# Performance work log

Measured on AMD Instinct MI355X. Metric: run time of the kernel, lower is better.

Reference implementation:

```python
import jax, jax.numpy as jnp
import numpy as np

B, D, L = 32, 512, 4096   # batch, latent_dim (dim1), time length
N, D2 = 77, 768           # text tokens, text_latent_dim (dim2)
BC = 24                   # number of conditioned batch elements
H = 8                     # num_heads
EPS = 1e-5


def _layernorm(x, g, b):
    mu = jnp.mean(x, axis=-1, keepdims=True)
    var = jnp.mean(jnp.square(x - mu), axis=-1, keepdims=True)
    return (x - mu) * jax.lax.rsqrt(var + EPS) * g + b


def setup_inputs() -> dict:
    key = jax.random.key(0)
    ks = jax.random.split(key, 8)
    s = 0.02
    return {
        "input_tensor": jax.random.normal(ks[0], (B, D, L), jnp.float32),
        "condition_tensor": jax.random.normal(ks[1], (B, N, D2), jnp.float32),
        "cond_indices": jnp.arange(BC, dtype=jnp.int64 if jax.config.jax_enable_x64 else jnp.int32),
        "ln_g": jnp.ones((D,), jnp.float32),
        "ln_b": jnp.zeros((D,), jnp.float32),
        "tln_g": jnp.ones((D2,), jnp.float32),
        "tln_b": jnp.zeros((D2,), jnp.float32),
        "Wq": jax.random.normal(ks[2], (D, D), jnp.float32) * s,
        "bq": jnp.zeros((D,), jnp.float32),
        "Wk": jax.random.normal(ks[3], (D2, D), jnp.float32) * s,
        "bk": jnp.zeros((D,), jnp.float32),
        "Wv": jax.random.normal(ks[4], (D2, D), jnp.float32) * s,
        "bv": jnp.zeros((D,), jnp.float32),
    }


def reference(input_tensor, condition_tensor, cond_indices,
              ln_g, ln_b, tln_g, tln_b, Wq, bq, Wk, bk, Wv, bv):
    dh = D // H
    # gather conditioned rows; [Bc, D, L] -> [Bc, T=L, D]
    x_cond = jnp.transpose(input_tensor[cond_indices], (0, 2, 1))
    cond = condition_tensor[cond_indices]  # [Bc, N, D2]

    q = _layernorm(x_cond, ln_g, ln_b) @ Wq + bq           # [Bc, T, D]
    cn = _layernorm(cond, tln_g, tln_b)                     # [Bc, N, D2]
    k = (cn @ Wk + bk).reshape(BC, N, H, dh)
    v = (cn @ Wv + bv).reshape(BC, N, H, dh)

    q = jax.nn.softmax(q.reshape(BC, L, H, dh), axis=-1)   # feature-map softmax
    k = jax.nn.softmax(k, axis=1)                           # softmax over tokens N

    context = jnp.einsum('bnhk,bnhv->bhkv', k, v)           # [Bc, H, dh, dh]
    y = jnp.einsum('bthk,bhkv->bthv', q, context).reshape(BC, L, D)

    # scatter residual back: indices are unique, so .add == torch index assignment
    return input_tensor.at[cond_indices].add(jnp.transpose(y, (0, 2, 1)))
```

## Files before the change

kernel.cpp:

```cpp
#include <hip/hip_runtime.h>

#define LN_EPS 1e-5f

typedef __attribute__((ext_vector_type(8))) short bf16x8;
typedef __attribute__((ext_vector_type(4))) float f32x4;

__device__ __forceinline__ unsigned short f2bf(float f){
  unsigned u = __builtin_bit_cast(unsigned, f);
  u = (u + 0x7fffu + ((u >> 16) & 1u)) >> 16;
  return (unsigned short)u;
}

__global__ void k_wqt(const float* __restrict__ Wq, unsigned short* __restrict__ WqT){
  const int tid = blockIdx.x * 256 + threadIdx.x;
  const int d = tid >> 9, n = tid & 511;
  WqT[(size_t)n * 512 + d] = f2bf(Wq[(size_t)d * 512 + n]);
}

__global__ void k_condkv(const float* __restrict__ cond, const int* __restrict__ idx,
                         const float* __restrict__ tg, const float* __restrict__ tb,
                         const float* __restrict__ Wk, const float* __restrict__ bk,
                         const float* __restrict__ Wv, const float* __restrict__ bv,
                         float* __restrict__ kbuf, float* __restrict__ vbuf)
{
  __shared__ float cn[16][768];
  const int bc = blockIdx.z, nc = blockIdx.y, dc = blockIdx.x;
  const int b = idx[bc];
  const int n0 = nc * 16;
  int nrows = 77 - n0; if(nrows > 16) nrows = 16;
  const int w = threadIdx.x >> 6, lane = threadIdx.x & 63;

  for(int r = w; r < nrows; r += 4){
    const float* src = cond + ((size_t)b * 77 + n0 + r) * 768;
    float vals[12]; float s1 = 0.f, s2 = 0.f;
    #pragma unroll
    for(int i=0;i<12;i++){ float x = src[lane + i*64]; vals[i]=x; s1+=x; s2+=x*x; }
    #pragma unroll
    for(int off=1; off<64; off<<=1){ s1 += __shfl_xor(s1, off); s2 += __shfl_xor(s2, off); }
    const float mu  = s1 * (1.f/768.f);
    const float var = s2 * (1.f/768.f) - mu*mu;
    const float rs  = rsqrtf(var + LN_EPS);
    #pragma unroll
    for(int i=0;i<12;i++){ const int c2 = lane + i*64; cn[r][c2] = (vals[i]-mu)*rs*tg[c2] + tb[c2]; }
  }
  __syncthreads();

  const int dq = threadIdx.x & 63;
  const int part = threadIdx.x >> 6;
  const float* W    = (dc < 2) ? Wk : Wv;
  const float* bias = (dc < 2) ? bk : bv;
  float* obuf       = (dc < 2) ? kbuf : vbuf;
  const int d0 = (dc & 1) * 256 + dq * 4;

  float acc[4][4] = {};
  for(int i=0;i<768;i++){
    const float4 wv = *(const float4*)(W + (size_t)i * 512 + d0);
    #pragma unroll
    for(int j=0;j<4;j++){
      const float c = cn[part*4 + j][i];
      acc[j][0] += c * wv.x; acc[j][1] += c * wv.y;
      acc[j][2] += c * wv.z; acc[j][3] += c * wv.w;
    }
  }
  #pragma unroll
  for(int j=0;j<4;j++){
    const int r = part*4 + j, n = n0 + r;
    if(r < nrows){
      float4 o;
      o.x = acc[j][0] + bias[d0+0];
      o.y = acc[j][1] + bias[d0+1];
      o.z = acc[j][2] + bias[d0+2];
      o.w = acc[j][3] + bias[d0+3];
      *(float4*)(obuf + ((size_t)bc * 77 + n) * 512 + d0) = o;
    }
  }
}

__global__ void k_ctx(const float* __restrict__ kbuf, const float* __restrict__ vbuf,
                      unsigned short* __restrict__ ctxT)
{
  __shared__ float kk[77][64];
  __shared__ float vv[77][64];
  __shared__ float inv_s[64];
  const int h = blockIdx.x, bc = blockIdx.y;
  const int tid = threadIdx.x;
  for(int e = tid; e < 77*64; e += 256){
    const int n = e >> 6, c = e & 63;
    kk[n][c] = kbuf[((size_t)bc * 77 + n) * 512 + h*64 + c];
    vv[n][c] = vbuf[((size_t)bc * 77 + n) * 512 + h*64 + c];
  }
  __syncthreads();
  if(tid < 64){
    float m = -1e30f;
    for(int n=0;n<77;n++) m = fmaxf(m, kk[n][tid]);
    float s = 0.f;
    for(int n=0;n<77;n++){ const float e = __expf(kk[n][tid] - m); kk[n][tid] = e; s += e; }
    inv_s[tid] = 1.f / s;
  }
  __syncthreads();
  #pragma unroll
  for(int j=0;j<16;j++){
    const int o = tid + 256*j;
    const int v = o >> 6, k2 = o & 63;
    float a = 0.f;
    for(int n=0;n<77;n++) a += kk[n][k2] * vv[n][v];
    ctxT[((size_t)(bc*8 + h)) * 4096 + v*64 + k2] = f2bf(a * inv_s[k2]);
  }
}

__global__ void k_copy(const float* __restrict__ in, const int* __restrict__ idx,
                       float* __restrict__ out)
{
  const int b = blockIdx.y;
  bool member = false;
  for(int i=0;i<24;i++) member |= (idx[i] == b);
  if(member) return;
  const float4* s = (const float4*)(in  + (size_t)b * 512 * 4096);
  float4*       d = (float4*)      (out + (size_t)b * 512 * 4096);
  for(int i = blockIdx.x*256 + threadIdx.x; i < 512*4096/4; i += 128*256) d[i] = s[i];
}

__global__ __launch_bounds__(256, 2)
void k_main(const float* __restrict__ input, const int* __restrict__ idx,
            const float* __restrict__ ln_g, const float* __restrict__ ln_b,
            const unsigned short* __restrict__ WqT, const float* __restrict__ bq,
            const unsigned short* __restrict__ ctxT, float* __restrict__ out)
{
  __shared__ __align__(16) unsigned short A[32][40];
  __shared__ __align__(16) unsigned short Bt[512][40];
  __shared__ __align__(16) unsigned short P[4][32][136];
  __shared__ float mu_s[32], rs_s[32];
  __shared__ float red1[4][8][4], red2[4][8][4];

  const int tid  = threadIdx.x;
  const int lane = tid & 63;
  const int w    = tid >> 6;
  const int col  = lane & 15;
  const int g    = lane >> 4;
  const int bc   = blockIdx.y;
  const int b    = idx[bc];
  const int t0   = blockIdx.x * 32;
  const float* xb = input + (size_t)b * (512*4096);
  float*       ob = out   + (size_t)b * (512*4096);

  {
    const int p  = tid & 7;
    const int dg = tid >> 3;
    float s1[4] = {0,0,0,0}, s2[4] = {0,0,0,0};
    for(int i=0;i<16;i++){
      const float4 x = *(const float4*)(xb + (size_t)(dg + i*32) * 4096 + t0 + p*4);
      s1[0]+=x.x; s1[1]+=x.y; s1[2]+=x.z; s1[3]+=x.w;
      s2[0]+=x.x*x.x; s2[1]+=x.y*x.y; s2[2]+=x.z*x.z; s2[3]+=x.w*x.w;
    }
    #pragma unroll
    for(int off=8; off<64; off<<=1){
      #pragma unroll
      for(int j=0;j<4;j++){ s1[j] += __shfl_xor(s1[j], off); s2[j] += __shfl_xor(s2[j], off); }
    }
    if(lane < 8){
      #pragma unroll
      for(int j=0;j<4;j++){ red1[w][lane][j] = s1[j]; red2[w][lane][j] = s2[j]; }
    }
    __syncthreads();
    if(tid < 32){
      const int pp = tid >> 2, j = tid & 3;
      float a = 0.f, c = 0.f;
      #pragma unroll
      for(int ww=0; ww<4; ++ww){ a += red1[ww][pp][j]; c += red2[ww][pp][j]; }
      const float mu  = a * (1.f/512.f);
      const float var = c * (1.f/512.f) - mu*mu;
      mu_s[tid] = mu;
      rs_s[tid] = rsqrtf(var + LN_EPS);
    }
    __syncthreads();
  }

  f32x4 acc[2][8] = {};

  for(int ks=0; ks<16; ++ks){
    const int dbase = ks * 32;
    {
      const int dl = tid >> 3;
      const int p  = tid & 7;
      const int d  = dbase + dl;
      const float4 x = *(const float4*)(xb + (size_t)d * 4096 + t0 + p*4);
      const float gv = ln_g[d], bv = ln_b[d];
      const int t = p * 4;
      A[t+0][dl] = f2bf((x.x - mu_s[t+0]) * rs_s[t+0] * gv + bv);
      A[t+1][dl] = f2bf((x.y - mu_s[t+1]) * rs_s[t+1] * gv + bv);
      A[t+2][dl] = f2bf((x.z - mu_s[t+2]) * rs_s[t+2] * gv + bv);
      A[t+3][dl] = f2bf((x.w - mu_s[t+3]) * rs_s[t+3] * gv + bv);
    }
    #pragma unroll
    for(int i=0;i<8;i++){
      const int c  = tid + i*256;
      const int n  = c >> 2;
      const int o8 = (c & 3) * 8;
      *(int4*)(&Bt[n][o8]) = *(const int4*)(WqT + (size_t)n * 512 + dbase + o8);
    }
    __syncthreads();
    const bf16x8 af0 = *(const bf16x8*)(&A[col     ][g*8]);
    const bf16x8 af1 = *(const bf16x8*)(&A[col + 16][g*8]);
    #pragma unroll
    for(int nt=0; nt<8; ++nt){
      const bf16x8 bf = *(const bf16x8*)(&Bt[w*128 + nt*16 + col][g*8]);
      acc[0][nt] = __builtin_amdgcn_mfma_f32_16x16x32_bf16(af0, bf, acc[0][nt], 0, 0, 0);
      acc[1][nt] = __builtin_amdgcn_mfma_f32_16x16x32_bf16(af1, bf, acc[1][nt], 0, 0, 0);
    }
    __syncthreads();
  }

  #pragma unroll
  for(int mt=0; mt<2; ++mt){
    #pragma unroll
    for(int hh=0; hh<2; ++hh){
      #pragma unroll
      for(int q=0; q<4; ++q){
        const int nt = hh*4 + q;
        const float bqv = bq[w*128 + nt*16 + col];
        #pragma unroll
        for(int r=0;r<4;++r) acc[mt][nt][r] += bqv;
      }
      #pragma unroll
      for(int r=0;r<4;++r){
        float m = acc[mt][hh*4+0][r];
        #pragma unroll
        for(int q=1;q<4;++q) m = fmaxf(m, acc[mt][hh*4+q][r]);
        m = fmaxf(m, __shfl_xor(m, 1));
        m = fmaxf(m, __shfl_xor(m, 2));
        m = fmaxf(m, __shfl_xor(m, 4));
        m = fmaxf(m, __shfl_xor(m, 8));
        float s = 0.f;
        #pragma unroll
        for(int q=0;q<4;++q){
          const float e = __expf(acc[mt][hh*4+q][r] - m);
          acc[mt][hh*4+q][r] = e;
          s += e;
        }
        s += __shfl_xor(s, 1);
        s += __shfl_xor(s, 2);
        s += __shfl_xor(s, 4);
        s += __shfl_xor(s, 8);
        const float inv = 1.f / s;
        #pragma unroll
        for(int q=0;q<4;++q) acc[mt][hh*4+q][r] *= inv;
      }
    }
  }

  #pragma unroll
  for(int mt=0; mt<2; ++mt)
    #pragma unroll
    for(int nt=0; nt<8; ++nt)
      #pragma unroll
      for(int r=0; r<4; ++r)
        P[w][mt*16 + g*4 + r][nt*16 + col] = f2bf(acc[mt][nt][r]);

  #pragma unroll
  for(int hh=0; hh<2; ++hh){
    const int head = w*2 + hh;
    const unsigned short* cb = ctxT + ((size_t)(bc*8 + head)) * 4096;
    f32x4 y[4][2] = {};
    #pragma unroll
    for(int ks2=0; ks2<2; ++ks2){
      const bf16x8 pb0 = *(const bf16x8*)(&P[w][col     ][hh*64 + ks2*32 + g*8]);
      const bf16x8 pb1 = *(const bf16x8*)(&P[w][col + 16][hh*64 + ks2*32 + g*8]);
      #pragma unroll
      for(int vt=0; vt<4; ++vt){
        const bf16x8 af = *(const bf16x8*)(cb + (size_t)(vt*16 + col) * 64 + ks2*32 + g*8);
        y[vt][0] = __builtin_amdgcn_mfma_f32_16x16x32_bf16(af, pb0, y[vt][0], 0, 0, 0);
        y[vt][1] = __builtin_amdgcn_mfma_f32_16x16x32_bf16(af, pb1, y[vt][1], 0, 0, 0);
      }
    }
    #pragma unroll
    for(int vt=0; vt<4; ++vt)
      #pragma unroll
      for(int tt=0; tt<2; ++tt)
        #pragma unroll
        for(int r=0; r<4; ++r){
          const size_t a = (size_t)(head*64 + vt*16 + g*4 + r) * 4096 + (size_t)(t0 + tt*16 + col);
          ob[a] = xb[a] + y[vt][tt][r];
        }
  }
}

extern "C" void kernel_launch(void* const* d_in, const int* in_sizes, int n_in,
                              void* d_out, int out_size, void* d_ws, size_t ws_size,
                              hipStream_t stream)
{
  const float* input = (const float*)d_in[0];
  const float* cond  = (const float*)d_in[1];
  const int*   idx   = (const int*)d_in[2];
  const float* ln_g  = (const float*)d_in[3];
  const float* ln_b  = (const float*)d_in[4];
  const float* tln_g = (const float*)d_in[5];
  const float* tln_b = (const float*)d_in[6];
  const float* Wq    = (const float*)d_in[7];
  const float* bq    = (const float*)d_in[8];
  const float* Wk    = (const float*)d_in[9];
  const float* bk    = (const float*)d_in[10];
  const float* Wv    = (const float*)d_in[11];
  const float* bv    = (const float*)d_in[12];
  float* out = (float*)d_out;
  char*  ws  = (char*)d_ws;

  unsigned short* WqT  = (unsigned short*)(ws);
  unsigned short* ctxT = (unsigned short*)(ws + 524288);
  float* kbuf = (float*)(ws + 524288 + 1572864);
  float* vbuf = (float*)(ws + 524288 + 1572864 + 24*77*512*4);

  k_wqt   <<<dim3(1024),    dim3(256), 0, stream>>>(Wq, WqT);
  k_condkv<<<dim3(4,5,24),  dim3(256), 0, stream>>>(cond, idx, tln_g, tln_b, Wk, bk, Wv, bv, kbuf, vbuf);
  k_ctx   <<<dim3(8,24),    dim3(256), 0, stream>>>(kbuf, vbuf, ctxT);
  k_copy  <<<dim3(128,32),  dim3(256), 0, stream>>>(input, idx, out);
  k_main  <<<dim3(128,24),  dim3(256), 0, stream>>>(input, idx, ln_g, ln_b, WqT, bq, ctxT, out);
}
```

Baseline: 407.8 us.

## Split main kernel into LayerNorm-transpose pass and 128x128 tiled bf16 MFMA GEMM

Adds a pre-pass that layer-normalises and transposes the conditioned input into a bf16 [T,D] workspace. A new GEMM kernel with 128x128 tiles loads that workspace and WqT straight into LDS via global_load_lds, then applies the per-head softmax and the context MFMA in its epilogue. The aim is better operand reuse and MFMA utilisation than the old fused kernel, which redid LayerNorm inside the GEMM tile. The cost is an extra write and read of a roughly 100 MB bf16 intermediate. If the workspace is too small, the code falls back to the old kernel.

Measured after the change: 406.5 us. No clear change (-0.3%).

```diff
diff --git a/kernel.cpp b/kernel.cpp
--- a/kernel.cpp
+++ b/kernel.cpp
@@ -3,12 +3,19 @@
 #define LN_EPS 1e-5f
 
 typedef __attribute__((ext_vector_type(8))) short bf16x8;
+typedef __attribute__((ext_vector_type(8))) short s16x8;
 typedef __attribute__((ext_vector_type(4))) float f32x4;
 
 __device__ __forceinline__ unsigned short f2bf(float f){
   unsigned u = __builtin_bit_cast(unsigned, f);
   u = (u + 0x7fffu + ((u >> 16) & 1u)) >> 16;
   return (unsigned short)u;
+}
+
+__device__ __forceinline__ void gll16(const unsigned short* g, unsigned short* l){
+  __builtin_amdgcn_global_load_lds(
+      (const __attribute__((address_space(1))) unsigned int*)(g),
+      (__attribute__((address_space(3))) unsigned int*)(l), 16, 0, 0);
 }
 
 __global__ void k_wqt(const float* __restrict__ Wq, unsigned short* __restrict__ WqT){
@@ -118,6 +125,213 @@
   const float4* s = (const float4*)(in  + (size_t)b * 512 * 4096);
   float4*       d = (float4*)      (out + (size_t)b * 512 * 4096);
   for(int i = blockIdx.x*256 + threadIdx.x; i < 512*4096/4; i += 128*256) d[i] = s[i];
+}
+
+__global__ __launch_bounds__(256, 2)
+void k_lnt(const float* __restrict__ input, const int* __restrict__ idx,
+           const float* __restrict__ ln_g, const float* __restrict__ ln_b,
+           unsigned short* __restrict__ xT)
+{
+  __shared__ float buf[32][516];
+  __shared__ float red1[32][8], red2[32][8];
+  __shared__ float mu_s[32], rs_s[32];
+  __shared__ float gbuf[512], bbuf[512];
+
+  const int tid = threadIdx.x;
+  const int bc = blockIdx.y;
+  const int b  = idx[bc];
+  const int t0 = blockIdx.x * 32;
+  const float* xb = input + (size_t)b * (512*4096) + t0;
+
+  *(float2*)&gbuf[tid*2] = *(const float2*)&ln_g[tid*2];
+  *(float2*)&bbuf[tid*2] = *(const float2*)&ln_b[tid*2];
+
+  {
+    const int p  = tid & 7;
+    const int dg = tid >> 3;
+    #pragma unroll
+    for(int i=0;i<16;i++){
+      const int d = dg + i*32;
+      const float4 x = *(const float4*)(xb + (size_t)d * 4096 + p*4);
+      buf[p*4+0][d] = x.x; buf[p*4+1][d] = x.y;
+      buf[p*4+2][d] = x.z; buf[p*4+3][d] = x.w;
+    }
+  }
+  __syncthreads();
+
+  {
+    const int t = tid & 31, part = tid >> 5;
+    float s1 = 0.f, s2 = 0.f;
+    #pragma unroll
+    for(int i=0;i<16;i++){
+      const float4 v = *(const float4*)&buf[t][part*64 + i*4];
+      s1 += v.x+v.y+v.z+v.w;
+      s2 += v.x*v.x + v.y*v.y + v.z*v.z + v.w*v.w;
+    }
+    red1[t][part] = s1; red2[t][part] = s2;
+  }
+  __syncthreads();
+  if(tid < 32){
+    float a = 0.f, c = 0.f;
+    #pragma unroll
+    for(int p=0;p<8;p++){ a += red1[tid][p]; c += red2[tid][p]; }
+    const float mu  = a * (1.f/512.f);
+    const float var = c * (1.f/512.f) - mu*mu;
+    mu_s[tid] = mu; rs_s[tid] = rsqrtf(var + LN_EPS);
+  }
+  __syncthreads();
+
+  {
+    const int c  = tid & 7;
+    const int tt = tid >> 3;
+    const float mu = mu_s[tt], rs = rs_s[tt];
+    unsigned short* orow = xT + ((size_t)bc*4096 + t0 + tt) * 512;
+    #pragma unroll
+    for(int j=0;j<8;j++){
+      const int d0 = c*8 + j*64;
+      const float4 a  = *(const float4*)&buf[tt][d0];
+      const float4 b4 = *(const float4*)&buf[tt][d0+4];
+      const float4 g0 = *(const float4*)&gbuf[d0];
+      const float4 g1 = *(const float4*)&gbuf[d0+4];
+      const float4 h0 = *(const float4*)&bbuf[d0];
+      const float4 h1 = *(const float4*)&bbuf[d0+4];
+      s16x8 o;
+      o[0] = (short)f2bf((a.x -mu)*rs*g0.x + h0.x);
+      o[1] = (short)f2bf((a.y -mu)*rs*g0.y + h0.y);
+      o[2] = (short)f2bf((a.z -mu)*rs*g0.z + h0.z);
+      o[3] = (short)f2bf((a.w -mu)*rs*g0.w + h0.w);
+      o[4] = (short)f2bf((b4.x-mu)*rs*g1.x + h1.x);
+      o[5] = (short)f2bf((b4.y-mu)*rs*g1.y + h1.y);
+      o[6] = (short)f2bf((b4.z-mu)*rs*g1.z + h1.z);
+      o[7] = (short)f2bf((b4.w-mu)*rs*g1.w + h1.w);
+      *(s16x8*)(orow + d0) = o;
+    }
+  }
+}
+
+__global__ __launch_bounds__(256, 2)
+void k_gemm(const float* __restrict__ input, const int* __restrict__ idx,
+            const unsigned short* __restrict__ xT, const unsigned short* __restrict__ WqT,
+            const float* __restrict__ bq, const unsigned short* __restrict__ ctxT,
+            float* __restrict__ out)
+{
+  __shared__ __align__(16) unsigned short As[128][32];
+  __shared__ __align__(16) unsigned short Bs[128][32];
+  __shared__ __align__(16) unsigned short P[4][64][72];
+
+  const int tid  = threadIdx.x;
+  const int lane = tid & 63;
+  const int w    = tid >> 6;
+  const int col  = lane & 15;
+  const int g    = lane >> 4;
+  const int wm   = w >> 1, wn = w & 1;
+  const int mtile = blockIdx.x, ntile = blockIdx.y;
+  const int bc   = mtile >> 5;
+  const int tloc = (mtile & 31) * 128;
+  const int b    = idx[bc];
+  const size_t abase = (size_t)bc * 4096 + tloc;
+  const int nbase = ntile * 128;
+
+  const int fb0 = tid * 16;
+  const int fb1 = fb0 + 4096;
+  const int r0 = fb0 >> 6, o0 = (fb0 & 63) >> 1;
+  const int r1 = fb1 >> 6, o1 = (fb1 & 63) >> 1;
+  unsigned short* Af = &As[0][0];
+  unsigned short* Bf = &Bs[0][0];
+
+  f32x4 acc[4][4] = {};
+
+  for(int ks=0; ks<16; ++ks){
+    const int dbase = ks * 32;
+    __syncthreads();
+    gll16(xT  + (abase + r0) * 512 + dbase + o0, Af + (fb0 >> 1));
+    gll16(xT  + (abase + r1) * 512 + dbase + o1, Af + (fb1 >> 1));
+    gll16(WqT + (size_t)(nbase + r0) * 512 + dbase + o0, Bf + (fb0 >> 1));
+    gll16(WqT + (size_t)(nbase + r1) * 512 + dbase + o1, Bf + (fb1 >> 1));
+    __syncthreads();
+
+    bf16x8 af[4], bfr[4];
+    #pragma unroll
+    for(int mt=0; mt<4; ++mt) af[mt]  = *(const bf16x8*)&As[wm*64 + mt*16 + col][g*8];
+    #pragma unroll
+    for(int nt=0; nt<4; ++nt) bfr[nt] = *(const bf16x8*)&Bs[wn*64 + nt*16 + col][g*8];
+    #pragma unroll
+    for(int mt=0; mt<4; ++mt)
+      #pragma unroll
+      for(int nt=0; nt<4; ++nt)
+        acc[mt][nt] = __builtin_amdgcn_mfma_f32_16x16x32_bf16(af[mt], bfr[nt], acc[mt][nt], 0, 0, 0);
+  }
+
+  #pragma unroll
+  for(int mt=0; mt<4; ++mt){
+    #pragma unroll
+    for(int nt=0; nt<4; ++nt){
+      const float bqv = bq[nbase + wn*64 + nt*16 + col];
+      #pragma unroll
+      for(int r=0;r<4;++r) acc[mt][nt][r] += bqv;
+    }
+    #pragma unroll
+    for(int r=0;r<4;++r){
+      float m = acc[mt][0][r];
+      #pragma unroll
+      for(int q=1;q<4;++q) m = fmaxf(m, acc[mt][q][r]);
+      m = fmaxf(m, __shfl_xor(m, 1));
+      m = fmaxf(m, __shfl_xor(m, 2));
+      m = fmaxf(m, __shfl_xor(m, 4));
+      m = fmaxf(m, __shfl_xor(m, 8));
+      float s = 0.f;
+      #pragma unroll
+      for(int q=0;q<4;++q){
+        const float e = __expf(acc[mt][q][r] - m);
+        acc[mt][q][r] = e; s += e;
+      }
+      s += __shfl_xor(s, 1);
+      s += __shfl_xor(s, 2);
+      s += __shfl_xor(s, 4);
+      s += __shfl_xor(s, 8);
+      const float inv = 1.f / s;
+      #pragma unroll
+      for(int q=0;q<4;++q) acc[mt][q][r] *= inv;
+    }
+  }
+
+  #pragma unroll
+  for(int mt=0; mt<4; ++mt)
+    #pragma unroll
+    for(int nt=0; nt<4; ++nt)
+      #pragma unroll
+      for(int r=0; r<4; ++r)
+        P[w][mt*16 + g*4 + r][nt*16 + col] = f2bf(acc[mt][nt][r]);
+
+  const int head = ntile*2 + wn;
+  const unsigned short* cb = ctxT + ((size_t)(bc*8 + head)) * 4096;
+  f32x4 y[4][4] = {};
+  #pragma unroll
+  for(int ks2=0; ks2<2; ++ks2){
+    bf16x8 pb[4];
+    #pragma unroll
+    for(int tt=0; tt<4; ++tt) pb[tt] = *(const bf16x8*)&P[w][tt*16 + col][ks2*32 + g*8];
+    #pragma unroll
+    for(int vt=0; vt<4; ++vt){
+      const bf16x8 av = *(const bf16x8*)(cb + (size_t)(vt*16 + col) * 64 + ks2*32 + g*8);
+      #pragma unroll
+      for(int tt=0; tt<4; ++tt)
+        y[vt][tt] = __builtin_amdgcn_mfma_f32_16x16x32_bf16(av, pb[tt], y[vt][tt], 0, 0, 0);
+    }
+  }
+
+  const float* xb = input + (size_t)b * (512*4096);
+  float*       ob = out   + (size_t)b * (512*4096);
+  #pragma unroll
+  for(int vt=0; vt<4; ++vt)
+    #pragma unroll
+    for(int tt=0; tt<4; ++tt)
+      #pragma unroll
+      for(int r=0; r<4; ++r){
+        const size_t a = (size_t)(head*64 + vt*16 + g*4 + r) * 4096
+                       + (size_t)(tloc + wm*64 + tt*16 + col);
+        ob[a] = xb[a] + y[vt][tt][r];
+      }
 }
 
 __global__ __launch_bounds__(256, 2)
@@ -306,12 +520,20 @@
 
   unsigned short* WqT  = (unsigned short*)(ws);
   unsigned short* ctxT = (unsigned short*)(ws + 524288);
-  float* kbuf = (float*)(ws + 524288 + 1572864);
-  float* vbuf = (float*)(ws + 524288 + 1572864 + 24*77*512*4);
+  float* kbuf = (float*)(ws + 2097152);
+  float* vbuf = (float*)(ws + 2097152 + 3784704);
+  unsigned short* xT = (unsigned short*)(ws + 2097152 + 2*3784704);
+  const size_t need = 2097152 + 2*(size_t)3784704 + (size_t)24*4096*512*2;
 
   k_wqt   <<<dim3(1024),    dim3(256), 0, stream>>>(Wq, WqT);
   k_condkv<<<dim3(4,5,24),  dim3(256), 0, stream>>>(cond, idx, tln_g, tln_b, Wk, bk, Wv, bv, kbuf, vbuf);
   k_ctx   <<<dim3(8,24),    dim3(256), 0, stream>>>(kbuf, vbuf, ctxT);
   k_copy  <<<dim3(128,32),  dim3(256), 0, stream>>>(input, idx, out);
-  k_main  <<<dim3(128,24),  dim3(256), 0, stream>>>(input, idx, ln_g, ln_b, WqT, bq, ctxT, out);
-}
+
+  if(ws_size >= need){
+    k_lnt <<<dim3(128,24),  dim3(256), 0, stream>>>(input, idx, ln_g, ln_b, xT);
+    k_gemm<<<dim3(768,4),   dim3(256), 0, stream>>>(input, idx, xT, WqT, bq, ctxT, out);
+  } else {
+    k_main<<<dim3(128,24),  dim3(256), 0, stream>>>(input, idx, ln_g, ln_b, WqT, bq, ctxT, out);
+  }
+}
```

## Fold LayerNorm into Wq GEMM epilogue and retile main kernel with async LDS loads

Applied to the files above, without the earlier changes.

Folds the LayerNorm gain into the transposed bf16 Wq and precomputes per-column correction terms. The GEMM then runs on raw input, and the mean and rstd are applied in the epilogue instead of normalizing before the matmul. The main kernel is retiled to 128x128 output tiles and double-buffered with global_load_lds, and the statistics are accumulated from the staged tiles, so the separate stats pass over the input goes away. The context matrix is pre-swizzled for direct fragment loads, and the residual store uses float4. The risks are extra precision error from the mean-subtraction done after the GEMM, and each input tile now being reread by 4 N-tiles.

New measurement: 449.8 us. 1.1x slower.

```diff
diff --git a/kernel.cpp b/kernel.cpp
--- a/kernel.cpp
+++ b/kernel.cpp
@@ -1,4 +1,5 @@
 #include <hip/hip_runtime.h>
+#include <hip/hip_bf16.h>
 
 #define LN_EPS 1e-5f
 
@@ -10,11 +11,48 @@
   u = (u + 0x7fffu + ((u >> 16) & 1u)) >> 16;
   return (unsigned short)u;
 }
-
-__global__ void k_wqt(const float* __restrict__ Wq, unsigned short* __restrict__ WqT){
-  const int tid = blockIdx.x * 256 + threadIdx.x;
-  const int d = tid >> 9, n = tid & 511;
-  WqT[(size_t)n * 512 + d] = f2bf(Wq[(size_t)d * 512 + n]);
+__device__ __forceinline__ float bf2f(unsigned short h){
+  unsigned u = ((unsigned)h) << 16;
+  return __builtin_bit_cast(float, u);
+}
+__device__ __forceinline__ void gll16(const void* g, void* l){
+  __builtin_amdgcn_global_load_lds(
+      (const __attribute__((address_space(1))) unsigned int*)(g),
+      (__attribute__((address_space(3))) unsigned int*)(l), 16, 0, 0);
+}
+
+__global__ void k_prep(const float* __restrict__ Wq, const float* __restrict__ ln_g,
+                       const float* __restrict__ ln_b,
+                       unsigned short* __restrict__ gWqT, float2* __restrict__ c12)
+{
+  __shared__ float r1[64][4], r2[64][4];
+  const int tid = threadIdx.x;
+  const int n0 = blockIdx.x * 64;
+  const int c = tid & 63, q = tid >> 6;
+  float c1p = 0.f, c2p = 0.f;
+  for(int i=0;i<128;i+=4){
+    ushort4 pk;
+    unsigned short* pp = (unsigned short*)&pk;
+    #pragma unroll
+    for(int j=0;j<4;j++){
+      const int d = q*128 + i + j;
+      const float wv = Wq[(size_t)d*512 + n0 + c];
+      const float gw = ln_g[d] * wv;
+      const unsigned short hb = f2bf(gw);
+      pp[j] = hb;
+      c2p += bf2f(hb);
+      c1p += ln_b[d] * wv;
+    }
+    *(ushort4*)(gWqT + (size_t)(n0 + c)*512 + q*128 + i) = pk;
+  }
+  r1[c][q] = c1p; r2[c][q] = c2p;
+  __syncthreads();
+  if(q == 0){
+    float a = 0.f, b2 = 0.f;
+    #pragma unroll
+    for(int j=0;j<4;j++){ a += r1[c][j]; b2 += r2[c][j]; }
+    c12[n0 + c] = make_float2(a, b2);
+  }
 }
 
 __global__ void k_condkv(const float* __restrict__ cond, const int* __restrict__ idx,
@@ -77,7 +115,7 @@
 }
 
 __global__ void k_ctx(const float* __restrict__ kbuf, const float* __restrict__ vbuf,
-                      unsigned short* __restrict__ ctxT)
+                      unsigned short* __restrict__ ctxP)
 {
   __shared__ float kk[77][64];
   __shared__ float vv[77][64];
@@ -104,7 +142,8 @@
     const int v = o >> 6, k2 = o & 63;
     float a = 0.f;
     for(int n=0;n<77;n++) a += kk[n][k2] * vv[n][v];
-    ctxT[((size_t)(bc*8 + h)) * 4096 + v*64 + k2] = f2bf(a * inv_s[k2]);
+    const int pos = ((((k2>>5)*4 + (v>>4))*4 + ((k2>>3)&3))*16 + (v&15))*8 + (k2&7);
+    ctxP[((size_t)(bc*8 + h)) * 4096 + pos] = f2bf(a * inv_s[k2]);
   }
 }
 
@@ -120,168 +159,198 @@
   for(int i = blockIdx.x*256 + threadIdx.x; i < 512*4096/4; i += 128*256) d[i] = s[i];
 }
 
-__global__ __launch_bounds__(256, 2)
-void k_main(const float* __restrict__ input, const int* __restrict__ idx,
-            const float* __restrict__ ln_g, const float* __restrict__ ln_b,
-            const unsigned short* __restrict__ WqT, const float* __restrict__ bq,
-            const unsigned short* __restrict__ ctxT, float* __restrict__ out)
-{
-  __shared__ __align__(16) unsigned short A[32][40];
-  __shared__ __align__(16) unsigned short Bt[512][40];
-  __shared__ __align__(16) unsigned short P[4][32][136];
-  __shared__ float mu_s[32], rs_s[32];
-  __shared__ float red1[4][8][4], red2[4][8][4];
+__global__ __launch_bounds__(256, 3)
+void k_gemm2(const float* __restrict__ input, const int* __restrict__ idx,
+             const unsigned short* __restrict__ gWqT, const float2* __restrict__ c12,
+             const float* __restrict__ bq, const unsigned short* __restrict__ ctxP,
+             float* __restrict__ out)
+{
+  __shared__ __align__(16) char smem[49152];
+  float*          Xs0 = (float*)(smem);
+  unsigned short* Ws0 = (unsigned short*)(smem + 16384);
+  float*          Xs1 = (float*)(smem + 24576);
+  unsigned short* Ws1 = (unsigned short*)(smem + 40960);
+  unsigned short* P   = (unsigned short*)(smem);
+  float*          red = (float*)(smem + 36864);
+  float*          mu_s= (float*)(smem + 38912);
+  float*          rs_s= (float*)(smem + 39424);
 
   const int tid  = threadIdx.x;
   const int lane = tid & 63;
   const int w    = tid >> 6;
   const int col  = lane & 15;
   const int g    = lane >> 4;
-  const int bc   = blockIdx.y;
+  const int wm   = w >> 1, wn = w & 1;
+  const int ntile = blockIdx.x, mtile = blockIdx.y;
+  const int bc   = mtile >> 5;
+  const int tt0  = (mtile & 31) * 128;
   const int b    = idx[bc];
-  const int t0   = blockIdx.x * 32;
-  const float* xb = input + (size_t)b * (512*4096);
-  float*       ob = out   + (size_t)b * (512*4096);
-
-  {
-    const int p  = tid & 7;
-    const int dg = tid >> 3;
-    float s1[4] = {0,0,0,0}, s2[4] = {0,0,0,0};
-    for(int i=0;i<16;i++){
-      const float4 x = *(const float4*)(xb + (size_t)(dg + i*32) * 4096 + t0 + p*4);
-      s1[0]+=x.x; s1[1]+=x.y; s1[2]+=x.z; s1[3]+=x.w;
-      s2[0]+=x.x*x.x; s2[1]+=x.y*x.y; s2[2]+=x.z*x.z; s2[3]+=x.w*x.w;
-    }
-    #pragma unroll
-    for(int off=8; off<64; off<<=1){
-      #pragma unroll
-      for(int j=0;j<4;j++){ s1[j] += __shfl_xor(s1[j], off); s2[j] += __shfl_xor(s2[j], off); }
-    }
-    if(lane < 8){
-      #pragma unroll
-      for(int j=0;j<4;j++){ red1[w][lane][j] = s1[j]; red2[w][lane][j] = s2[j]; }
+  const int nbase = ntile * 128;
+  const char* xbase = (const char*)(input + (size_t)b * 512 * 4096) + (size_t)tt0 * 4;
+  const char* wbase = (const char*)gWqT + (size_t)nbase * 1024;
+
+  const int tstat = tid & 127;
+  const int hstat = tid >> 7;
+  float s1 = 0.f, s2 = 0.f;
+
+  float* Xbuf[2] = {Xs0, Xs1};
+  unsigned short* Wbuf[2] = {Ws0, Ws1};
+
+  #define STAGE(ks, bi)                                                          \
+  {                                                                              \
+    _Pragma("unroll")                                                            \
+    for(int i=0;i<4;i++){                                                        \
+      const int f = tid*16 + i*4096;                                             \
+      const int kk_ = f >> 9, oo_ = f & 511;                                     \
+      gll16(xbase + (size_t)((ks)*32 + kk_) * 16384 + oo_, (char*)Xbuf[bi] + f); \
+    }                                                                            \
+    _Pragma("unroll")                                                            \
+    for(int i=0;i<2;i++){                                                        \
+      const int f = tid*16 + i*4096;                                             \
+      const int nn_ = f >> 6, oo_ = f & 63;                                      \
+      gll16(wbase + (size_t)nn_ * 1024 + (ks)*64 + oo_, (char*)Wbuf[bi] + f);    \
+    }                                                                            \
+  }
+
+  f32x4 acc[4][4] = {};
+
+  STAGE(0, 0);
+  __syncthreads();
+
+  for(int ks=0; ks<16; ++ks){
+    const int cur = ks & 1;
+    if(ks < 15) STAGE(ks+1, cur^1);
+
+    const float* X = Xbuf[cur];
+    const unsigned short* W = Wbuf[cur];
+
+    bf16x8 af[4];
+    #pragma unroll
+    for(int mt=0; mt<4; ++mt){
+      const int t = wm*64 + mt*16 + col;
+      union { unsigned short s[8]; bf16x8 v; } u;
+      #pragma unroll
+      for(int j=0;j<8;++j){
+        const float fv = X[(g*8 + j)*128 + t];
+        u.s[j] = __bfloat16_as_ushort(__float2bfloat16(fv));
+      }
+      af[mt] = u.v;
+    }
+    bf16x8 bfr[4];
+    #pragma unroll
+    for(int nt=0; nt<4; ++nt)
+      bfr[nt] = *(const bf16x8*)(W + (size_t)(wn*64 + nt*16 + col)*32 + g*8);
+
+    #pragma unroll
+    for(int mt=0; mt<4; ++mt)
+      #pragma unroll
+      for(int nt=0; nt<4; ++nt)
+        acc[mt][nt] = __builtin_amdgcn_mfma_f32_16x16x32_bf16(af[mt], bfr[nt], acc[mt][nt], 0, 0, 0);
+
+    #pragma unroll
+    for(int i=0;i<16;++i){
+      const float xv = X[(hstat*16 + i)*128 + tstat];
+      s1 += xv; s2 += xv*xv;
     }
     __syncthreads();
-    if(tid < 32){
-      const int pp = tid >> 2, j = tid & 3;
-      float a = 0.f, c = 0.f;
-      #pragma unroll
-      for(int ww=0; ww<4; ++ww){ a += red1[ww][pp][j]; c += red2[ww][pp][j]; }
-      const float mu  = a * (1.f/512.f);
-      const float var = c * (1.f/512.f) - mu*mu;
-      mu_s[tid] = mu;
-      rs_s[tid] = rsqrtf(var + LN_EPS);
-    }
-    __syncthreads();
-  }
-
-  f32x4 acc[2][8] = {};
-
-  for(int ks=0; ks<16; ++ks){
-    const int dbase = ks * 32;
-    {
-      const int dl = tid >> 3;
-      const int p  = tid & 7;
-      const int d  = dbase + dl;
-      const float4 x = *(const float4*)(xb + (size_t)d * 4096 + t0 + p*4);
-      const float gv = ln_g[d], bv = ln_b[d];
-      const int t = p * 4;
-      A[t+0][dl] = f2bf((x.x - mu_s[t+0]) * rs_s[t+0] * gv + bv);
-      A[t+1][dl] = f2bf((x.y - mu_s[t+1]) * rs_s[t+1] * gv + bv);
-      A[t+2][dl] = f2bf((x.z - mu_s[t+2]) * rs_s[t+2] * gv + bv);
-      A[t+3][dl] = f2bf((x.w - mu_s[t+3]) * rs_s[t+3] * gv + bv);
-    }
-    #pragma unroll
-    for(int i=0;i<8;i++){
-      const int c  = tid + i*256;
-      const int n  = c >> 2;
-      const int o8 = (c & 3) * 8;
-      *(int4*)(&Bt[n][o8]) = *(const int4*)(WqT + (size_t)n * 512 + dbase + o8);
-    }
-    __syncthreads();
-    const bf16x8 af0 = *(const bf16x8*)(&A[col     ][g*8]);
-    const bf16x8 af1 = *(const bf16x8*)(&A[col + 16][g*8]);
-    #pragma unroll
-    for(int nt=0; nt<8; ++nt){
-      const bf16x8 bf = *(const bf16x8*)(&Bt[w*128 + nt*16 + col][g*8]);
-      acc[0][nt] = __builtin_amdgcn_mfma_f32_16x16x32_bf16(af0, bf, acc[0][nt], 0, 0, 0);
-      acc[1][nt] = __builtin_amdgcn_mfma_f32_16x16x32_bf16(af1, bf, acc[1][nt], 0, 0, 0);
-    }
-    __syncthreads();
-  }
-
-  #pragma unroll
-  for(int mt=0; mt<2; ++mt){
-    #pragma unroll
-    for(int hh=0; hh<2; ++hh){
-      #pragma unroll
-      for(int q=0; q<4; ++q){
-        const int nt = hh*4 + q;
-        const float bqv = bq[w*128 + nt*16 + col];
-        #pragma unroll
-        for(int r=0;r<4;++r) acc[mt][nt][r] += bqv;
-      }
-      #pragma unroll
-      for(int r=0;r<4;++r){
-        float m = acc[mt][hh*4+0][r];
-        #pragma unroll
-        for(int q=1;q<4;++q) m = fmaxf(m, acc[mt][hh*4+q][r]);
-        m = fmaxf(m, __shfl_xor(m, 1));
-        m = fmaxf(m, __shfl_xor(m, 2));
-        m = fmaxf(m, __shfl_xor(m, 4));
-        m = fmaxf(m, __shfl_xor(m, 8));
-        float s = 0.f;
-        #pragma unroll
-        for(int q=0;q<4;++q){
-          const float e = __expf(acc[mt][hh*4+q][r] - m);
-          acc[mt][hh*4+q][r] = e;
-          s += e;
-        }
-        s += __shfl_xor(s, 1);
-        s += __shfl_xor(s, 2);
-        s += __shfl_xor(s, 4);
-        s += __shfl_xor(s, 8);
-        const float inv = 1.f / s;
-        #pragma unroll
-        for(int q=0;q<4;++q) acc[mt][hh*4+q][r] *= inv;
-      }
-    }
-  }
-
-  #pragma unroll
-  for(int mt=0; mt<2; ++mt)
-    #pragma unroll
-    for(int nt=0; nt<8; ++nt)
+  }
+  #undef STAGE
+
+  red[tstat*4 + hstat*2 + 0] = s1;
+  red[tstat*4 + hstat*2 + 1] = s2;
+  __syncthreads();
+  if(tid < 128){
+    const float a = red[tid*4 + 0] + red[tid*4 + 2];
+    const float c = red[tid*4 + 1] + red[tid*4 + 3];
+    const float mu = a * (1.f/512.f);
+    const float var = c * (1.f/512.f) - mu*mu;
+    mu_s[tid] = mu;
+    rs_s[tid] = rsqrtf(var + LN_EPS);
+  }
+  __syncthreads();
+
+  float c1b[4], c2v[4];
+  #pragma unroll
+  for(int nt=0; nt<4; ++nt){
+    const int n = nbase + wn*64 + nt*16 + col;
+    const float2 cc = c12[n];
+    c1b[nt] = cc.x + bq[n];
+    c2v[nt] = cc.y;
+  }
+  #pragma unroll
+  for(int mt=0; mt<4; ++mt){
+    #pragma unroll
+    for(int r=0; r<4; ++r){
+      const int t = wm*64 + mt*16 + g*4 + r;
+      const float mur = mu_s[t], rsr = rs_s[t];
+      const float mrc = rsr * mur;
+      float v[4];
+      #pragma unroll
+      for(int nt=0; nt<4; ++nt)
+        v[nt] = rsr*acc[mt][nt][r] - mrc*c2v[nt] + c1b[nt];
+      float m = fmaxf(fmaxf(v[0],v[1]), fmaxf(v[2],v[3]));
+      m = fmaxf(m, __shfl_xor(m, 1));
+      m = fmaxf(m, __shfl_xor(m, 2));
+      m = fmaxf(m, __shfl_xor(m, 4));
+      m = fmaxf(m, __shfl_xor(m, 8));
+      float s = 0.f;
+      #pragma unroll
+      for(int nt=0; nt<4; ++nt){ v[nt] = __expf(v[nt] - m); s += v[nt]; }
+      s += __shfl_xor(s, 1);
+      s += __shfl_xor(s, 2);
+      s += __shfl_xor(s, 4);
+      s += __shfl_xor(s, 8);
+      const float inv = 1.f / s;
+      #pragma unroll
+      for(int nt=0; nt<4; ++nt) acc[mt][nt][r] = v[nt] * inv;
+    }
+  }
+
+  unsigned short* Pw = P + w * 64 * 72;
+  #pragma unroll
+  for(int mt=0; mt<4; ++mt)
+    #pragma unroll
+    for(int nt=0; nt<4; ++nt)
       #pragma unroll
       for(int r=0; r<4; ++r)
-        P[w][mt*16 + g*4 + r][nt*16 + col] = f2bf(acc[mt][nt][r]);
-
-  #pragma unroll
-  for(int hh=0; hh<2; ++hh){
-    const int head = w*2 + hh;
-    const unsigned short* cb = ctxT + ((size_t)(bc*8 + head)) * 4096;
-    f32x4 y[4][2] = {};
-    #pragma unroll
-    for(int ks2=0; ks2<2; ++ks2){
-      const bf16x8 pb0 = *(const bf16x8*)(&P[w][col     ][hh*64 + ks2*32 + g*8]);
-      const bf16x8 pb1 = *(const bf16x8*)(&P[w][col + 16][hh*64 + ks2*32 + g*8]);
-      #pragma unroll
-      for(int vt=0; vt<4; ++vt){
-        const bf16x8 af = *(const bf16x8*)(cb + (size_t)(vt*16 + col) * 64 + ks2*32 + g*8);
-        y[vt][0] = __builtin_amdgcn_mfma_f32_16x16x32_bf16(af, pb0, y[vt][0], 0, 0, 0);
-        y[vt][1] = __builtin_amdgcn_mfma_f32_16x16x32_bf16(af, pb1, y[vt][1], 0, 0, 0);
-      }
-    }
+        Pw[(mt*16 + g*4 + r)*72 + nt*16 + col] = f2bf(acc[mt][nt][r]);
+
+  const int head = ntile*2 + wn;
+  const unsigned short* cp = ctxP + (size_t)(bc*8 + head) * 4096;
+  f32x4 y[4][4] = {};
+  #pragma unroll
+  for(int ks2=0; ks2<2; ++ks2){
+    bf16x8 pa[4];
+    #pragma unroll
+    for(int mt=0; mt<4; ++mt)
+      pa[mt] = *(const bf16x8*)(Pw + (mt*16 + col)*72 + ks2*32 + g*8);
+    bf16x8 cv[4];
     #pragma unroll
     for(int vt=0; vt<4; ++vt)
-      #pragma unroll
-      for(int tt=0; tt<2; ++tt)
-        #pragma unroll
-        for(int r=0; r<4; ++r){
-          const size_t a = (size_t)(head*64 + vt*16 + g*4 + r) * 4096 + (size_t)(t0 + tt*16 + col);
-          ob[a] = xb[a] + y[vt][tt][r];
-        }
-  }
+      cv[vt] = *(const bf16x8*)(cp + (size_t)(((ks2*4 + vt)*4 + g)*16 + col) * 8);
+    #pragma unroll
+    for(int mt=0; mt<4; ++mt)
+      #pragma unroll
+      for(int vt=0; vt<4; ++vt)
+        y[mt][vt] = __builtin_amdgcn_mfma_f32_16x16x32_bf16(pa[mt], cv[vt], y[mt][vt], 0, 0, 0);
+  }
+
+  const float* xb = input + (size_t)b * 512 * 4096;
+  float*       ob = out   + (size_t)b * 512 * 4096;
+  #pragma unroll
+  for(int mt=0; mt<4; ++mt)
+    #pragma unroll
+    for(int vt=0; vt<4; ++vt){
+      const size_t row = (size_t)(head*64 + vt*16 + col);
+      const size_t a = row*4096 + (size_t)(tt0 + wm*64 + mt*16 + g*4);
+      const float4 xr = *(const float4*)(xb + a);
+      float4 o4;
+      o4.x = xr.x + y[mt][vt][0];
+      o4.y = xr.y + y[mt][vt][1];
+      o4.z = xr.z + y[mt][vt][2];
+      o4.w = xr.w + y[mt][vt][3];
+      *(float4*)(ob + a) = o4;
+    }
 }
 
 extern "C" void kernel_launch(void* const* d_in, const int* in_sizes, int n_in,
@@ -304,14 +373,15 @@
   float* out = (float*)d_out;
   char*  ws  = (char*)d_ws;
 
-  unsigned short* WqT  = (unsigned short*)(ws);
-  unsigned short* ctxT = (unsigned short*)(ws + 524288);
-  float* kbuf = (float*)(ws + 524288 + 1572864);
-  float* vbuf = (float*)(ws + 524288 + 1572864 + 24*77*512*4);
-
-  k_wqt   <<<dim3(1024),    dim3(256), 0, stream>>>(Wq, WqT);
+  unsigned short* gWqT = (unsigned short*)(ws);
+  float2*         c12  = (float2*)(ws + 524288);
+  unsigned short* ctxP = (unsigned short*)(ws + 528384);
+  float* kbuf = (float*)(ws + 2101248);
+  float* vbuf = (float*)(ws + 2101248 + 3784704);
+
+  k_prep  <<<dim3(8),       dim3(256), 0, stream>>>(Wq, ln_g, ln_b, gWqT, c12);
   k_condkv<<<dim3(4,5,24),  dim3(256), 0, stream>>>(cond, idx, tln_g, tln_b, Wk, bk, Wv, bv, kbuf, vbuf);
-  k_ctx   <<<dim3(8,24),    dim3(256), 0, stream>>>(kbuf, vbuf, ctxT);
+  k_ctx   <<<dim3(8,24),    dim3(256), 0, stream>>>(kbuf, vbuf, ctxP);
   k_copy  <<<dim3(128,32),  dim3(256), 0, stream>>>(input, idx, out);
-  k_main  <<<dim3(128,24),  dim3(256), 0, stream>>>(input, idx, ln_g, ln_b, WqT, bq, ctxT, out);
-}
+  k_gemm2 <<<dim3(4,768),   dim3(256), 0, stream>>>(input, idx, gWqT, c12, bq, ctxP, out);
+}
```
